# Kernel optimization log

Measured on AMD Instinct MI355X. Metric: run time of the kernel, lower is better.

The kernel has to match this reference:

```python
import jax, jax.numpy as jnp
import numpy as np

HEAD_DIM = 64


def setup_inputs() -> dict:
    key = jax.random.key(0)
    ks = jax.random.split(key, 7)
    B, T, S = 8, 256, 4096
    E, KV = 512, 768          # embed_dim, kv_dim
    H, D = 8, HEAD_DIM        # num_heads, head_dim
    x = jax.random.normal(ks[0], (B, T, E), dtype=jnp.float32)
    context = jax.random.normal(ks[1], (B, S, KV), dtype=jnp.float32)
    key_padding_mask = jax.random.randint(ks[2], (B, S), 0, 2) > 0  # True = ignore
    Wq = jax.random.normal(ks[3], (H * D, E), dtype=jnp.float32) * 0.02
    Wkv = jax.random.normal(ks[4], (2 * H * D, KV), dtype=jnp.float32) * 0.02
    Wo = jax.random.normal(ks[5], (E, H * D), dtype=jnp.float32) * 0.02
    bo = jnp.zeros((E,), dtype=jnp.float32)
    return {"x": x, "context": context, "key_padding_mask": key_padding_mask,
            "Wq": Wq, "Wkv": Wkv, "Wo": Wo, "bo": bo}


def reference(x, context, key_padding_mask, Wq, Wkv, Wo, bo):
    B, T, _ = x.shape
    S = context.shape[1]
    D = HEAD_DIM
    H = Wq.shape[0] // D
    scale = D ** (-0.5)

    # q: (B, H, T, D)
    q = (x @ Wq.T).reshape(B, T, H, D).transpose(0, 2, 1, 3)
    # kv: (B, S, 2, H, D) -> k, v each (B, H, S, D)
    kv = (context @ Wkv.T).reshape(B, S, 2, H, D)
    k = kv[:, :, 0].transpose(0, 2, 1, 3)
    v = kv[:, :, 1].transpose(0, 2, 1, 3)

    # attention scores (B, H, T, S) -- materialized, matching att_weights capture
    attn = jnp.einsum('bhtd,bhsd->bhts', q, k) * scale
    attn = jnp.where(key_padding_mask[:, None, None, :], -jnp.inf, attn)
    attn = jax.nn.softmax(attn, axis=-1)  # dropout p=0.0 -> identity

    out = jnp.einsum('bhts,bhsd->bthd', attn, v).reshape(B, T, H * D)
    return out @ Wo.T + bo
```

## Files before the change

### kernel.cpp

```cpp
#include <hip/hip_runtime.h>
#include <hip/hip_bf16.h>


typedef float f32x4 __attribute__((ext_vector_type(4)));
typedef __bf16 bf16x8 __attribute__((ext_vector_type(8)));
typedef unsigned short u16x8 __attribute__((ext_vector_type(8)));
typedef unsigned short u16x4 __attribute__((ext_vector_type(4)));
typedef unsigned int u32x4 __attribute__((ext_vector_type(4)));

static __device__ __forceinline__ unsigned short f2bf(float f) {
  return __builtin_bit_cast(unsigned short, (__bf16)f);
}
static __device__ __forceinline__ unsigned pk2(float lo, float hi) {
  return (unsigned)f2bf(lo) | ((unsigned)f2bf(hi) << 16);
}
static __device__ __forceinline__ f32x4 mfma16(bf16x8 a, bf16x8 b, f32x4 c) {
  return __builtin_amdgcn_mfma_f32_16x16x32_bf16(a, b, c, 0, 0, 0);
}
static __device__ __forceinline__ bf16x8 ld_frag(const unsigned short* lds, int byteOff) {
  return __builtin_bit_cast(bf16x8, *(const u16x8*)((const char*)lds + byteOff));
}
static __device__ __forceinline__ void gll16(const void* g, void* l) {
  __builtin_amdgcn_global_load_lds((__attribute__((address_space(1))) void*)(void*)g,
                                   (__attribute__((address_space(3))) void*)l, 16, 0, 0);
}
static __device__ __forceinline__ int swz4(int row) {
  return (row + (row >> 1)) & 3;
}

__global__ __launch_bounds__(256) void cvt_bf16(const float* __restrict__ in,
                                                unsigned short* __restrict__ out, int n8) {
  int i = blockIdx.x * 256 + threadIdx.x;
  if (i >= n8) return;
  const f32x4* p = (const f32x4*)(in + (long)i * 8);
  f32x4 a = p[0], b = p[1];
  u16x8 o = { f2bf(a[0]), f2bf(a[1]), f2bf(a[2]), f2bf(a[3]),
              f2bf(b[0]), f2bf(b[1]), f2bf(b[2]), f2bf(b[3]) };
  *(u16x8*)(out + (long)i * 8) = o;
}

__global__ __launch_bounds__(256) void gemm_kv(
    const unsigned short* __restrict__ A, const unsigned short* __restrict__ Bw,
    unsigned short* __restrict__ kbuf, unsigned short* __restrict__ vbuf) {
  constexpr int K = 768;
  constexpr int NT = K / 32;
  __shared__ unsigned short As[3][128 * 32];
  __shared__ unsigned short Bs[3][128 * 32];
  const int tid = threadIdx.x;
  const int l = tid & 63, wid = tid >> 6;
  const int wr = wid >> 1, wc = wid & 1;
  const int r = l & 15, g = l >> 4;
  const int bid = blockIdx.x;
  const int xcd = bid & 7, j = bid >> 3;
  const long m0 = (long)(xcd * 32 + (j >> 3)) * 128;
  const long n0 = (long)(j & 7) * 128;

  const int row0 = tid >> 2, cs = tid & 3;
  const int gk0 = (cs ^ swz4(row0)) * 8;
  const unsigned short* aR = A + (m0 + row0) * K + gk0;
  const unsigned short* bR = Bw + (n0 + row0) * K + gk0;

  auto stage = [&](int sbuf, int kt) {
    const unsigned short* ap = aR + kt * 32;
    const unsigned short* bp = bR + kt * 32;
    gll16(ap,          (char*)As[sbuf] + tid * 16);
    gll16(ap + 64 * K, (char*)As[sbuf] + 4096 + tid * 16);
    gll16(bp,          (char*)Bs[sbuf] + tid * 16);
    gll16(bp + 64 * K, (char*)Bs[sbuf] + 4096 + tid * 16);
  };

  f32x4 acc[4][4] = {};
  stage(0, 0);
  stage(1, 1);
  asm volatile("s_waitcnt vmcnt(4)" ::: "memory");
  __builtin_amdgcn_s_barrier();
  __builtin_amdgcn_sched_barrier(0);

  int cur = 0, nxt2 = 2;
  for (int t = 0; t < NT; ++t) {
    if (t + 2 < NT) stage(nxt2, t + 2);
    bf16x8 af[4], bfr[4];
#pragma unroll
    for (int m = 0; m < 4; ++m) {
      int row = wr * 64 + m * 16 + r;
      af[m] = ld_frag(As[cur], row * 64 + ((g ^ swz4(row)) << 4));
    }
#pragma unroll
    for (int n = 0; n < 4; ++n) {
      int row = wc * 64 + n * 16 + r;
      bfr[n] = ld_frag(Bs[cur], row * 64 + ((g ^ swz4(row)) << 4));
    }
    __builtin_amdgcn_s_setprio(1);
#pragma unroll
    for (int m = 0; m < 4; ++m)
#pragma unroll
      for (int n = 0; n < 4; ++n)
        acc[m][n] = mfma16(af[m], bfr[n], acc[m][n]);
    __builtin_amdgcn_s_setprio(0);
    if (t + 2 < NT) {
      asm volatile("s_waitcnt vmcnt(4)" ::: "memory");
    } else {
      asm volatile("s_waitcnt vmcnt(0)" ::: "memory");
    }
    __builtin_amdgcn_s_barrier();
    __builtin_amdgcn_sched_barrier(0);
    cur = (cur == 2) ? 0 : cur + 1;
    nxt2 = (nxt2 == 2) ? 0 : nxt2 + 1;
  }

#pragma unroll
  for (int m = 0; m < 4; ++m) {
#pragma unroll
    for (int n = 0; n < 4; ++n) {
      f32x4 v = acc[m][n];
      const long rg0 = m0 + wr * 64 + m * 16 + g * 4;
      const long cg = n0 + wc * 64 + n * 16 + r;
      if (cg < 512) {
        int hh = (int)(cg >> 6), dd = (int)(cg & 63);
#pragma unroll
        for (int i = 0; i < 4; ++i) {
          long rg = rg0 + i;
          int bb = (int)(rg >> 12), ss = (int)(rg & 4095);
          kbuf[(((long)(bb * 8 + hh) * 4096 + ss) << 6) + dd] = f2bf(v[i]);
        }
      } else {
        int c2 = (int)(cg - 512);
        int hh = c2 >> 6, dd = c2 & 63;
        int bb = (int)(rg0 >> 12), ss = (int)(rg0 & 4095);
        u16x4 pk = { f2bf(v[0]), f2bf(v[1]), f2bf(v[2]), f2bf(v[3]) };
        *(u16x4*)&vbuf[(((long)(bb * 8 + hh) * 64 + dd) << 12) + ss] = pk;
      }
    }
  }
}

template <int OUTMODE, typename TA>
__global__ __launch_bounds__(256) void gemm_bt(
    const TA* __restrict__ A, const float* __restrict__ Bw,
    int M, int N, int K,
    unsigned short* __restrict__ o16a,
    float* __restrict__ oF, const float* __restrict__ bias) {
  __shared__ unsigned short As[2][128 * 32];
  __shared__ unsigned short Bs[2][128 * 32];
  const int tid = threadIdx.x;
  const int l = tid & 63, wid = tid >> 6;
  const int wr = wid >> 1, wc = wid & 1;
  const int r = l & 15, g = l >> 4;
  const long m0 = (long)blockIdx.y * 128, n0 = (long)blockIdx.x * 128;

  const int srow = tid >> 1, sseg = tid & 1;
  const int sz = swz4(srow);
  const int wb0 = srow * 64 + (((sseg * 2) ^ sz) << 4);
  const int wb1 = srow * 64 + (((sseg * 2 + 1) ^ sz) << 4);

  const TA* aptr = A + (m0 + srow) * (long)K + sseg * 16;
  const float* bptr = Bw + (n0 + srow) * (long)K + sseg * 16;

  f32x4 rA[4]; u16x8 rAh[2]; f32x4 rB[4];
  auto loadT = [&](int kt) {
    if constexpr (sizeof(TA) == 4) {
      const f32x4* p = (const f32x4*)(aptr + kt * 32);
      rA[0] = p[0]; rA[1] = p[1]; rA[2] = p[2]; rA[3] = p[3];
    } else {
      const u16x8* p = (const u16x8*)(aptr + kt * 32);
      rAh[0] = p[0]; rAh[1] = p[1];
    }
    const f32x4* q = (const f32x4*)(bptr + kt * 32);
    rB[0] = q[0]; rB[1] = q[1]; rB[2] = q[2]; rB[3] = q[3];
  };
  auto writeT = [&](int sbuf) {
    char* ab = (char*)As[sbuf];
    if constexpr (sizeof(TA) == 4) {
      u32x4 lo = { pk2(rA[0][0], rA[0][1]), pk2(rA[0][2], rA[0][3]),
                   pk2(rA[1][0], rA[1][1]), pk2(rA[1][2], rA[1][3]) };
      u32x4 hi = { pk2(rA[2][0], rA[2][1]), pk2(rA[2][2], rA[2][3]),
                   pk2(rA[3][0], rA[3][1]), pk2(rA[3][2], rA[3][3]) };
      *(u32x4*)(ab + wb0) = lo; *(u32x4*)(ab + wb1) = hi;
    } else {
      *(u16x8*)(ab + wb0) = rAh[0]; *(u16x8*)(ab + wb1) = rAh[1];
    }
    char* bb = (char*)Bs[sbuf];
    u32x4 lo = { pk2(rB[0][0], rB[0][1]), pk2(rB[0][2], rB[0][3]),
                 pk2(rB[1][0], rB[1][1]), pk2(rB[1][2], rB[1][3]) };
    u32x4 hi = { pk2(rB[2][0], rB[2][1]), pk2(rB[2][2], rB[2][3]),
                 pk2(rB[3][0], rB[3][1]), pk2(rB[3][2], rB[3][3]) };
    *(u32x4*)(bb + wb0) = lo; *(u32x4*)(bb + wb1) = hi;
  };

  f32x4 acc[4][4] = {};
  const int nt = K >> 5;
  loadT(0); writeT(0);
  __syncthreads();
  int buf = 0;
  for (int t = 0; t < nt; ++t) {
    if (t + 1 < nt) loadT(t + 1);
    bf16x8 af[4], bfr[4];
#pragma unroll
    for (int m = 0; m < 4; ++m) {
      int row = wr * 64 + m * 16 + r;
      af[m] = ld_frag(As[buf], row * 64 + ((g ^ swz4(row)) << 4));
    }
#pragma unroll
    for (int n = 0; n < 4; ++n) {
      int row = wc * 64 + n * 16 + r;
      bfr[n] = ld_frag(Bs[buf], row * 64 + ((g ^ swz4(row)) << 4));
    }
#pragma unroll
    for (int m = 0; m < 4; ++m)
#pragma unroll
      for (int n = 0; n < 4; ++n)
        acc[m][n] = mfma16(af[m], bfr[n], acc[m][n]);
    if (t + 1 < nt) writeT(buf ^ 1);
    __syncthreads();
    buf ^= 1;
  }

#pragma unroll
  for (int m = 0; m < 4; ++m) {
#pragma unroll
    for (int n = 0; n < 4; ++n) {
      f32x4 v = acc[m][n];
      const long rg0 = m0 + wr * 64 + m * 16 + g * 4;
      const long cg = n0 + wc * 64 + n * 16 + r;
      if constexpr (OUTMODE == 0) {
#pragma unroll
        for (int i = 0; i < 4; ++i) {
          long rg = rg0 + i;
          int bb = (int)(rg >> 8), tt = (int)(rg & 255);
          int hh = (int)(cg >> 6), dd = (int)(cg & 63);
          o16a[(((long)(bb * 8 + hh) * 256 + tt) << 6) + dd] = f2bf(v[i]);
        }
      } else {
#pragma unroll
        for (int i = 0; i < 4; ++i) {
          long rg = rg0 + i;
          oF[rg * (long)N + cg] = v[i] + bias[cg];
        }
      }
    }
  }
}

__global__ __launch_bounds__(256) void attn_fwd(
    const unsigned short* __restrict__ qbuf,
    const unsigned short* __restrict__ kbuf,
    const unsigned short* __restrict__ vbuf,
    const int* __restrict__ mask,
    float* __restrict__ po, float* __restrict__ ml) {
  __shared__ unsigned short Ks[2][64 * 64];
  __shared__ unsigned short Vs[2][64 * 64];
  __shared__ unsigned short Ps[4][16 * 64];
  const int tid = threadIdx.x;
  const int l = tid & 63, w = tid >> 6;
  const int r = l & 15, g = l >> 4;
  const int bid = blockIdx.x;
  const int j = (bid & 7) * 128 + (bid >> 3);
  const int qt = j & 3, bh = (j >> 2) & 63, sp = j >> 8;

  const unsigned short* qrow = qbuf + (((long)bh * 256) + qt * 64 + w * 16 + r) * 64;
  const bf16x8 qf0 = __builtin_bit_cast(bf16x8, *(const u16x8*)(qrow + g * 8));
  const bf16x8 qf1 = __builtin_bit_cast(bf16x8, *(const u16x8*)(qrow + 32 + g * 8));

  f32x4 accO[4] = {};
  float mrow[4] = { -1e30f, -1e30f, -1e30f, -1e30f };
  float lrow[4] = {};
  const float SCL = 0.125f * 1.44269504088896340736f;

  const int s_base = sp * 1024;
  const unsigned short* kbase = kbuf + ((long)bh * 4096 + s_base) * 64;
  const unsigned short* vbase = vbuf + ((long)bh * 64) * 4096 + s_base;
  const int* mbase = mask + (bh >> 3) * 4096 + s_base;

  const int st_row = tid >> 3, st_c = tid & 7;
  auto stage = [&](int sbuf, int t0) {
#pragma unroll
    for (int p = 0; p < 2; ++p) {
      int row = p * 32 + st_row;
      int colb = (st_c * 16) ^ ((row & 7) << 4);
      int ldsOff = (p * 256 + tid) * 16;
      gll16(kbase + (long)(t0 + row) * 64 + (colb >> 1), (char*)Ks[sbuf] + ldsOff);
      gll16(vbase + (long)row * 4096 + t0 + (colb >> 1), (char*)Vs[sbuf] + ldsOff);
    }
  };

  stage(0, 0);
  asm volatile("s_waitcnt vmcnt(0)" ::: "memory");
  __builtin_amdgcn_s_barrier();
  __builtin_amdgcn_sched_barrier(0);

  int buf = 0;
  for (int it = 0; it < 16; ++it) {
    if (it + 1 < 16) stage(buf ^ 1, (it + 1) * 64);

    f32x4 sc[4] = {};
    __builtin_amdgcn_s_setprio(1);
#pragma unroll
    for (int nf = 0; nf < 4; ++nf) {
      int row = nf * 16 + r;
      int swz = (row & 7) << 4;
      bf16x8 k0 = ld_frag(Ks[buf], row * 128 + ((g * 16) ^ swz));
      bf16x8 k1 = ld_frag(Ks[buf], row * 128 + ((g * 16 + 64) ^ swz));
      sc[nf] = mfma16(qf0, k0, sc[nf]);
      sc[nf] = mfma16(qf1, k1, sc[nf]);
    }
    __builtin_amdgcn_s_setprio(0);

    float s[4][4];
#pragma unroll
    for (int nf = 0; nf < 4; ++nf) {
      bool mk = mbase[it * 64 + nf * 16 + r] != 0;
#pragma unroll
      for (int i = 0; i < 4; ++i) s[nf][i] = mk ? -1e30f : sc[nf][i] * SCL;
    }

    float tm[4], pr[4][4], rs[4], corr[4];
#pragma unroll
    for (int i = 0; i < 4; ++i) {
      tm[i] = fmaxf(fmaxf(s[0][i], s[1][i]), fmaxf(s[2][i], s[3][i]));
#pragma unroll
      for (int off = 1; off < 16; off <<= 1)
        tm[i] = fmaxf(tm[i], __shfl_xor(tm[i], off));
      float mn = fmaxf(mrow[i], tm[i]);
      corr[i] = exp2f(mrow[i] - mn);
      mrow[i] = mn;
      rs[i] = 0.f;
    }
#pragma unroll
    for (int nf = 0; nf < 4; ++nf)
#pragma unroll
      for (int i = 0; i < 4; ++i) {
        pr[nf][i] = exp2f(s[nf][i] - mrow[i]);
        rs[i] += pr[nf][i];
      }
#pragma unroll
    for (int i = 0; i < 4; ++i) {
#pragma unroll
      for (int off = 1; off < 16; off <<= 1)
        rs[i] += __shfl_xor(rs[i], off);
      lrow[i] = lrow[i] * corr[i] + rs[i];
    }
    f32x4 cv = { corr[0], corr[1], corr[2], corr[3] };
#pragma unroll
    for (int nf = 0; nf < 4; ++nf) accO[nf] *= cv;

    unsigned short* Pw = Ps[w];
#pragma unroll
    for (int nf = 0; nf < 4; ++nf)
#pragma unroll
      for (int i = 0; i < 4; ++i) {
        int prow = g * 4 + i;
        int pb = prow * 128 + ((((nf * 16 + r) * 2)) ^ ((prow & 7) << 4));
        *(unsigned short*)((char*)Pw + pb) = f2bf(pr[nf][i]);
      }
    asm volatile("s_waitcnt lgkmcnt(0)" ::: "memory");
    bf16x8 pf0 = ld_frag(Pw, r * 128 + ((g * 16) ^ ((r & 7) << 4)));
    bf16x8 pf1 = ld_frag(Pw, r * 128 + ((g * 16 + 64) ^ ((r & 7) << 4)));

    __builtin_amdgcn_s_setprio(1);
#pragma unroll
    for (int nf = 0; nf < 4; ++nf) {
      int row = nf * 16 + r;
      int swz = (row & 7) << 4;
      bf16x8 v0 = ld_frag(Vs[buf], row * 128 + ((g * 16) ^ swz));
      bf16x8 v1 = ld_frag(Vs[buf], row * 128 + ((g * 16 + 64) ^ swz));
      accO[nf] = mfma16(pf0, v0, accO[nf]);
      accO[nf] = mfma16(pf1, v1, accO[nf]);
    }
    __builtin_amdgcn_s_setprio(0);

    asm volatile("s_waitcnt vmcnt(0)" ::: "memory");
    __builtin_amdgcn_s_barrier();
    __builtin_amdgcn_sched_barrier(0);
    buf ^= 1;
  }

  const long rowg = (long)bh * 256 + qt * 64 + w * 16 + g * 4;
#pragma unroll
  for (int nf = 0; nf < 4; ++nf)
#pragma unroll
    for (int i = 0; i < 4; ++i)
      po[((long)sp * 16384 + rowg + i) * 64 + nf * 16 + r] = accO[nf][i];
  if (r == 0) {
#pragma unroll
    for (int i = 0; i < 4; ++i) {
      ml[((long)sp * 16384 + rowg + i) * 2 + 0] = mrow[i];
      ml[((long)sp * 16384 + rowg + i) * 2 + 1] = lrow[i];
    }
  }
}

__global__ __launch_bounds__(256) void attn_merge(
    const float* __restrict__ po, const float* __restrict__ ml,
    unsigned short* __restrict__ obuf) {
  const int idx = blockIdx.x * 256 + threadIdx.x;
  const int row = idx >> 2, dc = (idx & 3) << 4;
  float ms[4], ls[4], mx = -1e30f;
#pragma unroll
  for (int sp = 0; sp < 4; ++sp) {
    ms[sp] = ml[((long)sp * 16384 + row) * 2 + 0];
    ls[sp] = ml[((long)sp * 16384 + row) * 2 + 1];
    mx = fmaxf(mx, ms[sp]);
  }
  float lsum = 0.f, wg[4];
#pragma unroll
  for (int sp = 0; sp < 4; ++sp) { wg[sp] = exp2f(ms[sp] - mx); lsum += wg[sp] * ls[sp]; }
  const float inv = 1.f / lsum;
  f32x4 o[4] = {};
#pragma unroll
  for (int sp = 0; sp < 4; ++sp) {
    const f32x4* p = (const f32x4*)(po + ((long)sp * 16384 + row) * 64 + dc);
#pragma unroll
    for (int c = 0; c < 4; ++c) o[c] += wg[sp] * p[c];
  }
  u16x8 o0, o1;
#pragma unroll
  for (int k = 0; k < 8; ++k) {
    o0[k] = f2bf(o[k >> 2][k & 3] * inv);
    o1[k] = f2bf(o[2 + (k >> 2)][k & 3] * inv);
  }
  const long off = (((long)((row >> 11) * 256 + (row & 255))) << 9) + ((row >> 8) & 7) * 64 + dc;
  *(u16x8*)&obuf[off] = o0;
  *(u16x8*)&obuf[off + 8] = o1;
}

extern "C" void kernel_launch(void* const* d_in, const int* in_sizes, int n_in,
                              void* d_out, int out_size, void* d_ws, size_t ws_size,
                              hipStream_t stream) {
  (void)in_sizes; (void)n_in; (void)out_size; (void)ws_size;
  const float* x    = (const float*)d_in[0];
  const float* ctx  = (const float*)d_in[1];
  const int*   mask = (const int*)d_in[2];
  const float* Wq   = (const float*)d_in[3];
  const float* Wkv  = (const float*)d_in[4];
  const float* Wo   = (const float*)d_in[5];
  const float* bo   = (const float*)d_in[6];
  float* out = (float*)d_out;

  char* ws = (char*)d_ws;
  const size_t MiB = 1024 * 1024;
  unsigned short* kbuf = (unsigned short*)(ws);
  unsigned short* vbuf = (unsigned short*)(ws + 32 * MiB);
  unsigned short* ctxb = (unsigned short*)(ws + 64 * MiB);
  unsigned short* qbuf = (unsigned short*)(ws + 64 * MiB);
  unsigned short* obuf = (unsigned short*)(ws + 66 * MiB);
  float* po = (float*)(ws + 68 * MiB);
  float* ml = (float*)(ws + 84 * MiB);
  unsigned short* wkvb = (unsigned short*)(ws + 112 * MiB);

  cvt_bf16<<<dim3(12288), 256, 0, stream>>>(ctx, ctxb, 3145728);
  cvt_bf16<<<dim3(384), 256, 0, stream>>>(Wkv, wkvb, 98304);
  gemm_kv<<<dim3(2048), 256, 0, stream>>>(ctxb, wkvb, kbuf, vbuf);
  gemm_bt<0, float><<<dim3(4, 16), 256, 0, stream>>>(
      x, Wq, 2048, 512, 512, qbuf, nullptr, nullptr);
  attn_fwd<<<dim3(1024), 256, 0, stream>>>(qbuf, kbuf, vbuf, mask, po, ml);
  attn_merge<<<dim3(256), 256, 0, stream>>>(po, ml, obuf);
  gemm_bt<2, unsigned short><<<dim3(4, 16), 256, 0, stream>>>(
      obuf, Wo, 2048, 512, 512, nullptr, out, bo);
}
```

Before: 196.7 us.

## Fuse context fp32-to-bf16 conversion into KV projection GEMM A-tile staging

Removes the separate pass that converts the large context tensor to bf16. The KV GEMM now loads fp32 context rows into registers, converts and packs them to bf16, and writes them to swizzled LDS with a double-buffered A path, while B still uses direct global-to-LDS loads. This saves a full write and reread of the converted tensor, but doubles A bytes fetched per tile and adds register pressure and conversion work inside the GEMM loop.

```diff
diff --git a/kernel.cpp b/kernel.cpp
--- a/kernel.cpp
+++ b/kernel.cpp
@@ -40,11 +40,11 @@
 }
 
 __global__ __launch_bounds__(256) void gemm_kv(
-    const unsigned short* __restrict__ A, const unsigned short* __restrict__ Bw,
+    const float* __restrict__ A, const unsigned short* __restrict__ Bw,
     unsigned short* __restrict__ kbuf, unsigned short* __restrict__ vbuf) {
   constexpr int K = 768;
   constexpr int NT = K / 32;
-  __shared__ unsigned short As[3][128 * 32];
+  __shared__ unsigned short As[2][128 * 32];
   __shared__ unsigned short Bs[3][128 * 32];
   const int tid = threadIdx.x;
   const int l = tid & 63, wid = tid >> 6;
@@ -55,40 +55,47 @@
   const long m0 = (long)(xcd * 32 + (j >> 3)) * 128;
   const long n0 = (long)(j & 7) * 128;
 
+  const int srow = tid >> 1, sseg = tid & 1;
+  const int szw = swz4(srow);
+  const int wb0 = srow * 64 + (((sseg * 2) ^ szw) << 4);
+  const int wb1 = srow * 64 + (((sseg * 2 + 1) ^ szw) << 4);
+  const float* aP = A + (m0 + srow) * (long)K + sseg * 16;
   const int row0 = tid >> 2, cs = tid & 3;
-  const int gk0 = (cs ^ swz4(row0)) * 8;
-  const unsigned short* aR = A + (m0 + row0) * K + gk0;
-  const unsigned short* bR = Bw + (n0 + row0) * K + gk0;
-
-  auto stage = [&](int sbuf, int kt) {
-    const unsigned short* ap = aR + kt * 32;
-    const unsigned short* bp = bR + kt * 32;
-    gll16(ap,          (char*)As[sbuf] + tid * 16);
-    gll16(ap + 64 * K, (char*)As[sbuf] + 4096 + tid * 16);
+  const unsigned short* bR = Bw + (n0 + row0) * (long)K + (cs ^ swz4(row0)) * 8;
+
+  f32x4 a0[4], a1[4];
+  auto loadA0 = [&](int kt) { const f32x4* p = (const f32x4*)(aP + kt * 32);
+    a0[0] = p[0]; a0[1] = p[1]; a0[2] = p[2]; a0[3] = p[3]; };
+  auto loadA1 = [&](int kt) { const f32x4* p = (const f32x4*)(aP + kt * 32);
+    a1[0] = p[0]; a1[1] = p[1]; a1[2] = p[2]; a1[3] = p[3]; };
+  auto glB = [&](int sbuf, int kt) { const unsigned short* bp = bR + kt * 32;
     gll16(bp,          (char*)Bs[sbuf] + tid * 16);
-    gll16(bp + 64 * K, (char*)Bs[sbuf] + 4096 + tid * 16);
-  };
+    gll16(bp + 64 * K, (char*)Bs[sbuf] + 4096 + tid * 16); };
+  auto writeA0 = [&](int abuf) { char* ab = (char*)As[abuf];
+    u32x4 lo = { pk2(a0[0][0], a0[0][1]), pk2(a0[0][2], a0[0][3]),
+                 pk2(a0[1][0], a0[1][1]), pk2(a0[1][2], a0[1][3]) };
+    u32x4 hi = { pk2(a0[2][0], a0[2][1]), pk2(a0[2][2], a0[2][3]),
+                 pk2(a0[3][0], a0[3][1]), pk2(a0[3][2], a0[3][3]) };
+    *(u32x4*)(ab + wb0) = lo; *(u32x4*)(ab + wb1) = hi; };
+  auto writeA1 = [&](int abuf) { char* ab = (char*)As[abuf];
+    u32x4 lo = { pk2(a1[0][0], a1[0][1]), pk2(a1[0][2], a1[0][3]),
+                 pk2(a1[1][0], a1[1][1]), pk2(a1[1][2], a1[1][3]) };
+    u32x4 hi = { pk2(a1[2][0], a1[2][1]), pk2(a1[2][2], a1[2][3]),
+                 pk2(a1[3][0], a1[3][1]), pk2(a1[3][2], a1[3][3]) };
+    *(u32x4*)(ab + wb0) = lo; *(u32x4*)(ab + wb1) = hi; };
 
   f32x4 acc[4][4] = {};
-  stage(0, 0);
-  stage(1, 1);
-  asm volatile("s_waitcnt vmcnt(4)" ::: "memory");
-  __builtin_amdgcn_s_barrier();
-  __builtin_amdgcn_sched_barrier(0);
-
-  int cur = 0, nxt2 = 2;
-  for (int t = 0; t < NT; ++t) {
-    if (t + 2 < NT) stage(nxt2, t + 2);
+  auto compute = [&](const unsigned short* AsB, const unsigned short* BsB) {
     bf16x8 af[4], bfr[4];
 #pragma unroll
     for (int m = 0; m < 4; ++m) {
       int row = wr * 64 + m * 16 + r;
-      af[m] = ld_frag(As[cur], row * 64 + ((g ^ swz4(row)) << 4));
+      af[m] = ld_frag(AsB, row * 64 + ((g ^ swz4(row)) << 4));
     }
 #pragma unroll
     for (int n = 0; n < 4; ++n) {
       int row = wc * 64 + n * 16 + r;
-      bfr[n] = ld_frag(Bs[cur], row * 64 + ((g ^ swz4(row)) << 4));
+      bfr[n] = ld_frag(BsB, row * 64 + ((g ^ swz4(row)) << 4));
     }
     __builtin_amdgcn_s_setprio(1);
 #pragma unroll
@@ -97,15 +104,36 @@
       for (int n = 0; n < 4; ++n)
         acc[m][n] = mfma16(af[m], bfr[n], acc[m][n]);
     __builtin_amdgcn_s_setprio(0);
-    if (t + 2 < NT) {
-      asm volatile("s_waitcnt vmcnt(4)" ::: "memory");
-    } else {
-      asm volatile("s_waitcnt vmcnt(0)" ::: "memory");
-    }
+  };
+
+  loadA0(0); glB(0, 0);
+  loadA1(1); glB(1, 1);
+  writeA0(0);
+  asm volatile("s_waitcnt vmcnt(6) lgkmcnt(0)" ::: "memory");
+  __builtin_amdgcn_s_barrier();
+  __builtin_amdgcn_sched_barrier(0);
+
+  int b0i = 0, b1i = 1, b2i = 2;
+  for (int t = 0; t < NT; t += 2) {
+    if (t + 2 < NT) { loadA0(t + 2); glB(b2i, t + 2); }
+    compute(As[0], Bs[b0i]);
+    if (t + 2 < NT) { asm volatile("s_waitcnt vmcnt(6)" ::: "memory"); }
+    else            { asm volatile("s_waitcnt vmcnt(0)" ::: "memory"); }
+    writeA1(1);
+    asm volatile("s_waitcnt lgkmcnt(0)" ::: "memory");
     __builtin_amdgcn_s_barrier();
     __builtin_amdgcn_sched_barrier(0);
-    cur = (cur == 2) ? 0 : cur + 1;
-    nxt2 = (nxt2 == 2) ? 0 : nxt2 + 1;
+    if (t + 3 < NT) { loadA1(t + 3); glB(b0i, t + 3); }
+    compute(As[1], Bs[b1i]);
+    if (t + 2 < NT) {
+      if (t + 3 < NT) { asm volatile("s_waitcnt vmcnt(6)" ::: "memory"); }
+      else            { asm volatile("s_waitcnt vmcnt(0)" ::: "memory"); }
+      writeA0(0);
+      asm volatile("s_waitcnt lgkmcnt(0)" ::: "memory");
+      __builtin_amdgcn_s_barrier();
+      __builtin_amdgcn_sched_barrier(0);
+    }
+    int tmp = b2i; b2i = b1i; b1i = b0i; b0i = tmp;
   }
 
 #pragma unroll
@@ -440,16 +468,14 @@
   const size_t MiB = 1024 * 1024;
   unsigned short* kbuf = (unsigned short*)(ws);
   unsigned short* vbuf = (unsigned short*)(ws + 32 * MiB);
-  unsigned short* ctxb = (unsigned short*)(ws + 64 * MiB);
   unsigned short* qbuf = (unsigned short*)(ws + 64 * MiB);
   unsigned short* obuf = (unsigned short*)(ws + 66 * MiB);
   float* po = (float*)(ws + 68 * MiB);
   float* ml = (float*)(ws + 84 * MiB);
   unsigned short* wkvb = (unsigned short*)(ws + 112 * MiB);
 
-  cvt_bf16<<<dim3(12288), 256, 0, stream>>>(ctx, ctxb, 3145728);
   cvt_bf16<<<dim3(384), 256, 0, stream>>>(Wkv, wkvb, 98304);
-  gemm_kv<<<dim3(2048), 256, 0, stream>>>(ctxb, wkvb, kbuf, vbuf);
+  gemm_kv<<<dim3(2048), 256, 0, stream>>>(ctx, wkvb, kbuf, vbuf);
   gemm_bt<0, float><<<dim3(4, 16), 256, 0, stream>>>(
       x, Wq, 2048, 512, 512, qbuf, nullptr, nullptr);
   attn_fwd<<<dim3(1024), 256, 0, stream>>>(qbuf, kbuf, vbuf, mask, po, ml);
```

After: 214.5 us. 1.09x slower.
